# Kernel optimization log

Measured on AMD Instinct MI355X. Metric: run time of the kernel, lower is better.

## Reference

```python
import jax, jax.numpy as jnp
import numpy as np

B, S, D_MODEL, H, D = 2, 2048, 1024, 16, 64
SCALE = 1.0 / float(np.sqrt(D))


def setup_inputs() -> dict:
    key = jax.random.key(0)
    ks = jax.random.split(key, 5)
    x = jax.random.normal(ks[0], (B, S, D_MODEL), jnp.float32)
    qkv_w = jax.random.normal(ks[1], (3 * H * D, D_MODEL), jnp.float32) * 0.02
    out_w = jax.random.normal(ks[2], (D_MODEL, H * D), jnp.float32) * 0.02
    bias_p = jax.random.uniform(ks[3], (H, 1, 1), jnp.float32) * 2.0  # torch.rand(...)*2
    bias_a = jax.random.uniform(ks[4], (H, 1, 1), jnp.float32)
    # standard geometric RoPE frequencies over d_head//2 = 32 channels
    rope_freqs = 10000.0 ** (-jnp.arange(D // 2, dtype=jnp.float32) / (D // 2))
    return {"x": x, "qkv_w": qkv_w, "out_w": out_w,
            "bias_p": bias_p, "bias_a": bias_a, "rope_freqs": rope_freqs}


def _rope(t, c, s):
    # t: [B,H,S,d]; c,s: [1,1,S,d/2]. Split-half rotation as in apply_rope.
    d2 = t.shape[-1] // 2
    t1, t2 = t[..., :d2], t[..., d2:]
    return jnp.concatenate([t1 * c - t2 * s, t1 * s + t2 * c], axis=-1)


def reference(x, qkv_w, out_w, bias_p, bias_a, rope_freqs):
    Bb, Ss, _ = x.shape
    qkv = (x @ qkv_w.T).reshape(Bb, Ss, 3, H, D)
    q = qkv[:, :, 0].transpose(0, 2, 1, 3)  # [B,H,S,d]
    k = qkv[:, :, 1].transpose(0, 2, 1, 3)
    v = qkv[:, :, 2].transpose(0, 2, 1, 3)
    pos = jnp.arange(Ss, dtype=jnp.float32)
    ang = pos[:, None] * rope_freqs[None, :]                 # [S, d/2]
    c = jnp.cos(ang)[None, None]
    s = jnp.sin(ang)[None, None]
    q = _rope(q, c, s)
    k = _rope(k, c, s)
    scores = jnp.einsum('bhqd,bhkd->bhqk', q, k) * SCALE     # [B,H,S,S]
    p = jnp.maximum(bias_p, 0.01)                            # clamp(min=0.01)
    a = jnp.maximum(bias_a, 0.01)
    dist = jnp.abs(pos[None, :] - pos[:, None])              # [S,S]
    kb = -p * jnp.log1p(a * dist)                            # [H,S,S]
    attn = jax.nn.softmax(scores + kb[None], axis=-1)
    out = jnp.einsum('bhqk,bhkd->bhqd', attn, v)             # [B,H,S,d]
    out = out.transpose(0, 2, 1, 3).reshape(Bb, Ss, H * D)
    return out @ out_w.T
```

## Files before the change

### kernel.cpp

```cpp
#include <hip/hip_runtime.h>
#include <math.h>

#define BATCH  2
#define SEQ    2048
#define DMODEL 1024
#define NH     16
#define HD     64
#define NQKV   3072
#define ROWS   (BATCH*SEQ)

typedef unsigned short u16;
typedef __bf16 bf16x8 __attribute__((ext_vector_type(8)));
typedef float  f32x4  __attribute__((ext_vector_type(4)));

typedef const __attribute__((address_space(1))) void* gptr_t;
typedef __attribute__((address_space(3))) void* lptr_t;

__device__ __forceinline__ void gload16(lptr_t l, const void* g) {
    __builtin_amdgcn_global_load_lds((gptr_t)g, l, 16, 0, 0);
}

__device__ __forceinline__ u16 f2bf(float f) {
    unsigned int u = __float_as_uint(f);
    u += 0x7FFFu + ((u >> 16) & 1u);
    return (u16)(u >> 16);
}
__device__ __forceinline__ float bf2f(u16 v) {
    return __uint_as_float(((unsigned int)v) << 16);
}

__global__ void f2bf_kernel(const float* __restrict__ in, u16* __restrict__ out, int n)
{
    int i = (blockIdx.x * 256 + threadIdx.x) * 4;
    if (i >= n) return;
    float4 v = *(const float4*)(in + i);
    u16 o[4] = { f2bf(v.x), f2bf(v.y), f2bf(v.z), f2bf(v.w) };
    *(uint2*)(out + i) = *(const uint2*)o;
}

__global__ void bias_table_kernel(const float* __restrict__ bias_p,
                                  const float* __restrict__ bias_a,
                                  float* __restrict__ kb)
{
    int idx = blockIdx.x * 256 + threadIdx.x;
    int h = idx >> 11;
    int d = idx & (SEQ - 1);
    float p = fmaxf(bias_p[h], 0.01f);
    float a = fmaxf(bias_a[h], 0.01f);
    kb[idx] = -p * log1pf(a * (float)d);
}

__global__ void rope_table_kernel(const float* __restrict__ freqs, float* __restrict__ tab)
{
    int idx = blockIdx.x * 256 + threadIdx.x;
    int s = idx >> 5, d = idx & 31;
    float sn, cs;
    sincosf((float)s * freqs[d], &sn, &cs);
    tab[idx * 2]     = cs;
    tab[idx * 2 + 1] = sn;
}

template<bool BF16OUT>
__global__ __launch_bounds__(256) void gemm_bf16(
    const u16* __restrict__ A, const u16* __restrict__ B,
    void* __restrict__ Cout, int M, int N, int K)
{
    __shared__ __align__(16) u16 As[128][32];
    __shared__ __align__(16) u16 Bs[128][32];
    const int tid  = threadIdx.x;
    const int wave = tid >> 6, lane = tid & 63;
    const int quad = lane >> 4, l16 = lane & 15;
    const int wrow = (wave >> 1) * 64, wcol = (wave & 1) * 64;
    const int bm = blockIdx.x * 128, bn = blockIdx.y * 128;

    const int srow = lane >> 2;
    const int scol = ((lane & 3) ^ (srow & 3)) * 8;
    const int fsw = (quad ^ (l16 & 3)) * 8;

    f32x4 acc[4][4];
#pragma unroll
    for (int i = 0; i < 4; ++i)
#pragma unroll
        for (int j = 0; j < 4; ++j) acc[i][j] = (f32x4){0.f,0.f,0.f,0.f};

    const u16* Ag0 = A + (size_t)(bm + wave*32 + srow)      * K + scol;
    const u16* Ag1 = A + (size_t)(bm + wave*32 + 16 + srow) * K + scol;
    const u16* Bg0 = B + (size_t)(bn + wave*32 + srow)      * K + scol;
    const u16* Bg1 = B + (size_t)(bn + wave*32 + 16 + srow) * K + scol;

    for (int k0 = 0; k0 < K; k0 += 32) {
        __syncthreads();
        gload16((lptr_t)&As[wave*32][0],      Ag0 + k0);
        gload16((lptr_t)&As[wave*32 + 16][0], Ag1 + k0);
        gload16((lptr_t)&Bs[wave*32][0],      Bg0 + k0);
        gload16((lptr_t)&Bs[wave*32 + 16][0], Bg1 + k0);
        __syncthreads();
        bf16x8 af[4], bfr[4];
#pragma unroll
        for (int i = 0; i < 4; ++i)
            af[i] = *(const bf16x8*)&As[wrow + i*16 + l16][fsw];
#pragma unroll
        for (int j = 0; j < 4; ++j)
            bfr[j] = *(const bf16x8*)&Bs[wcol + j*16 + l16][fsw];
#pragma unroll
        for (int i = 0; i < 4; ++i)
#pragma unroll
            for (int j = 0; j < 4; ++j)
                acc[i][j] = __builtin_amdgcn_mfma_f32_16x16x32_bf16(af[i], bfr[j], acc[i][j], 0, 0, 0);
    }

#pragma unroll
    for (int i = 0; i < 4; ++i)
#pragma unroll
        for (int j = 0; j < 4; ++j) {
            int col = bn + wcol + j*16 + l16;
#pragma unroll
            for (int r = 0; r < 4; ++r) {
                int row = bm + wrow + i*16 + quad*4 + r;
                if (BF16OUT) ((u16*)Cout)[(size_t)row * N + col] = f2bf(acc[i][j][r]);
                else         ((float*)Cout)[(size_t)row * N + col] = acc[i][j][r];
            }
        }
}

__global__ __launch_bounds__(256) void qkv_convert(
    const u16* __restrict__ qkv_bf, const float* __restrict__ cs_tab,
    u16* __restrict__ Qb, u16* __restrict__ Kb, u16* __restrict__ Vt)
{
    __shared__ __align__(16) u16 Vtile[64][72];
    const int tid = threadIdx.x;
    const int r = tid >> 2, c = tid & 3;
    const int s0 = blockIdx.x * 64, h = blockIdx.y, b = blockIdx.z;
    const int s = s0 + r;
    const u16* src = qkv_bf + (size_t)(b * SEQ + s) * NQKV + h * HD;
    const size_t hb = (size_t)(b * NH + h) * SEQ * HD;

    *(uint4*)&Vtile[r][c*16]     = *(const uint4*)(src + 2*NH*HD + c*16);
    *(uint4*)&Vtile[r][c*16 + 8] = *(const uint4*)(src + 2*NH*HD + c*16 + 8);

    {
        const u16* m = src + ((c < 2) ? 0 : NH*HD);
        const int d1 = (c & 1) * 16;
        u16 x1[16], x2[16];
        *(uint4*)&x1[0] = *(const uint4*)(m + d1);
        *(uint4*)&x1[8] = *(const uint4*)(m + d1 + 8);
        *(uint4*)&x2[0] = *(const uint4*)(m + d1 + 32);
        *(uint4*)&x2[8] = *(const uint4*)(m + d1 + 40);
        const float* ct = cs_tab + ((size_t)s * 32 + d1) * 2;
        const float sc = (c < 2) ? 0.125f : 1.0f;
        u16 y1[16], y2[16];
#pragma unroll
        for (int u = 0; u < 16; ++u) {
            float cs = ct[u*2], sn = ct[u*2 + 1];
            float a = bf2f(x1[u]), bq = bf2f(x2[u]);
            y1[u] = f2bf((a * cs - bq * sn) * sc);
            y2[u] = f2bf((a * sn + bq * cs) * sc);
        }
        u16* dst = ((c < 2) ? Qb : Kb) + hb + (size_t)s * HD + d1;
        *(uint4*)(dst)      = *(const uint4*)&y1[0];
        *(uint4*)(dst + 8)  = *(const uint4*)&y1[8];
        *(uint4*)(dst + 32) = *(const uint4*)&y2[0];
        *(uint4*)(dst + 40) = *(const uint4*)&y2[8];
    }
    __syncthreads();

    u16 vv[16];
#pragma unroll
    for (int u = 0; u < 16; ++u) vv[u] = Vtile[c*16 + u][r];
    u16* dst = Vt + hb + (size_t)r * SEQ + s0 + c*16;
    *(uint4*)(dst)     = *(const uint4*)&vv[0];
    *(uint4*)(dst + 8) = *(const uint4*)&vv[8];
}

__global__ __launch_bounds__(256) void attn_mfma(
    const u16* __restrict__ Qb, const u16* __restrict__ Kb,
    const u16* __restrict__ Vt, const float* __restrict__ kbt,
    u16* __restrict__ attn_bf)
{
    __shared__ __align__(16) u16 Ks[64][64];
    __shared__ __align__(16) u16 Vs[64][64];
    __shared__ __align__(16) u16 Ps[64][72];
    __shared__ float bs_[128];

    const int tid = threadIdx.x;
    const int wave = tid >> 6, lane = tid & 63;
    const int quad = lane >> 4, l16 = lane & 15;
    const int q0 = blockIdx.x * 64, h = blockIdx.y, b = blockIdx.z;

    const u16* Qh = Qb + (size_t)(b * NH + h) * SEQ * HD;
    const u16* Kh = Kb + (size_t)(b * NH + h) * SEQ * HD;
    const u16* Vh = Vt + (size_t)(b * NH + h) * HD * SEQ;
    const float* kbh = kbt + h * SEQ;

    const int qrow = q0 + wave * 16 + l16;
    const bf16x8 qf0 = *(const bf16x8*)(Qh + (size_t)qrow * HD + quad * 8);
    const bf16x8 qf1 = *(const bf16x8*)(Qh + (size_t)qrow * HD + 32 + quad * 8);

    const int srow = lane >> 3;
    const int scol = ((lane & 7) ^ srow) * 8;
    const u16* Kg0 = Kh + (size_t)(wave*16 + srow)     * HD + scol;
    const u16* Kg1 = Kh + (size_t)(wave*16 + 8 + srow) * HD + scol;
    const u16* Vg0 = Vh + (size_t)(wave*16 + srow)     * SEQ + scol;
    const u16* Vg1 = Vh + (size_t)(wave*16 + 8 + srow) * SEQ + scol;
    const int sw = (quad ^ (l16 & 7)) * 8;

    float l_part[4] = {0.f, 0.f, 0.f, 0.f};
    f32x4 o[4];
#pragma unroll
    for (int j = 0; j < 4; ++j) o[j] = (f32x4){0.f,0.f,0.f,0.f};

    for (int kt = 0; kt < SEQ / 64; ++kt) {
        const int k0 = kt * 64;
        __syncthreads();
        gload16((lptr_t)&Ks[wave*16][0],     Kg0 + (size_t)k0 * HD);
        gload16((lptr_t)&Ks[wave*16 + 8][0], Kg1 + (size_t)k0 * HD);
        gload16((lptr_t)&Vs[wave*16][0],     Vg0 + k0);
        gload16((lptr_t)&Vs[wave*16 + 8][0], Vg1 + k0);
        int dq = q0 - k0; if (dq < 0) dq = -dq;
        const int lo = (dq <= 63) ? 0 : dq - 63;
        if (tid < 128) {
            int idx = lo + tid;
            bs_[tid] = kbh[idx < SEQ ? idx : SEQ - 1];
        }
        __syncthreads();

        f32x4 sc[4];
#pragma unroll
        for (int j = 0; j < 4; ++j) {
            bf16x8 kf0 = *(const bf16x8*)&Ks[j*16 + l16][sw];
            bf16x8 kf1 = *(const bf16x8*)&Ks[j*16 + l16][sw ^ 32];
            f32x4 z = (f32x4){0.f,0.f,0.f,0.f};
            z = __builtin_amdgcn_mfma_f32_16x16x32_bf16(qf0, kf0, z, 0, 0, 0);
            sc[j] = __builtin_amdgcn_mfma_f32_16x16x32_bf16(qf1, kf1, z, 0, 0, 0);
        }

#pragma unroll
        for (int r = 0; r < 4; ++r) {
            const int qidx = q0 + wave * 16 + quad * 4 + r;
            float e[4];
#pragma unroll
            for (int j = 0; j < 4; ++j) {
                int kidx = k0 + j * 16 + l16;
                int dist = qidx - kidx; if (dist < 0) dist = -dist;
                e[j] = __expf(sc[j][r] + bs_[dist - lo]);
                Ps[wave*16 + quad*4 + r][j*16 + l16] = f2bf(e[j]);
            }
            l_part[r] += (e[0] + e[1]) + (e[2] + e[3]);
        }

        bf16x8 pf0 = *(const bf16x8*)&Ps[wave*16 + l16][quad*8];
        bf16x8 pf1 = *(const bf16x8*)&Ps[wave*16 + l16][32 + quad*8];
#pragma unroll
        for (int j = 0; j < 4; ++j) {
            bf16x8 vf0 = *(const bf16x8*)&Vs[j*16 + l16][sw];
            bf16x8 vf1 = *(const bf16x8*)&Vs[j*16 + l16][sw ^ 32];
            o[j] = __builtin_amdgcn_mfma_f32_16x16x32_bf16(pf0, vf0, o[j], 0, 0, 0);
            o[j] = __builtin_amdgcn_mfma_f32_16x16x32_bf16(pf1, vf1, o[j], 0, 0, 0);
        }
    }

#pragma unroll
    for (int r = 0; r < 4; ++r) {
#pragma unroll
        for (int off = 1; off < 16; off <<= 1)
            l_part[r] += __shfl_xor(l_part[r], off);
        float inv = 1.0f / l_part[r];
        int row = q0 + wave * 16 + quad * 4 + r;
        u16* dst = attn_bf + (size_t)(b * SEQ + row) * DMODEL + h * HD;
#pragma unroll
        for (int j = 0; j < 4; ++j)
            dst[j*16 + l16] = f2bf(o[j][r] * inv);
    }
}

extern "C" void kernel_launch(void* const* d_in, const int* in_sizes, int n_in,
                              void* d_out, int out_size, void* d_ws, size_t ws_size,
                              hipStream_t stream)
{
    (void)in_sizes; (void)n_in; (void)out_size; (void)ws_size;
    const float* x      = (const float*)d_in[0];
    const float* qkv_w  = (const float*)d_in[1];
    const float* out_w  = (const float*)d_in[2];
    const float* bias_p = (const float*)d_in[3];
    const float* bias_a = (const float*)d_in[4];
    const float* freqs  = (const float*)d_in[5];
    float* out = (float*)d_out;

    char* ws = (char*)d_ws;
    u16*   qkv_bf  = (u16*)ws;
    u16*   attn_bf = (u16*)ws;
    u16*   x_bf    = (u16*)(ws + 25165824);
    u16*   Qb      = x_bf;
    u16*   w1_bf   = (u16*)(ws + 33554432);
    u16*   w2_bf   = (u16*)(ws + 39845888);
    u16*   Kb      = (u16*)(ws + 41943040);
    u16*   Vt      = (u16*)(ws + 50331648);
    float* kbt     = (float*)(ws + 58720256);
    float* cs_tab  = (float*)(ws + 58720256 + 131072);

    f2bf_kernel<<<dim3(ROWS*DMODEL/1024), 256, 0, stream>>>(x, x_bf, ROWS*DMODEL);
    f2bf_kernel<<<dim3(NQKV*DMODEL/1024), 256, 0, stream>>>(qkv_w, w1_bf, NQKV*DMODEL);
    f2bf_kernel<<<dim3(DMODEL*DMODEL/1024), 256, 0, stream>>>(out_w, w2_bf, DMODEL*DMODEL);
    rope_table_kernel<<<dim3(SEQ*32/256), 256, 0, stream>>>(freqs, cs_tab);
    bias_table_kernel<<<dim3(NH*SEQ/256), 256, 0, stream>>>(bias_p, bias_a, kbt);

    gemm_bf16<true><<<dim3(ROWS/128, NQKV/128), 256, 0, stream>>>(x_bf, w1_bf, qkv_bf, ROWS, NQKV, DMODEL);
    qkv_convert<<<dim3(SEQ/64, NH, BATCH), 256, 0, stream>>>(qkv_bf, cs_tab, Qb, Kb, Vt);
    attn_mfma<<<dim3(SEQ/64, NH, BATCH), 256, 0, stream>>>(Qb, Kb, Vt, kbt, attn_bf);
    gemm_bf16<false><<<dim3(ROWS/128, DMODEL/128), 256, 0, stream>>>(attn_bf, w2_bf, out, ROWS, DMODEL, DMODEL);
}
```

Before: 248.3 us.

## Restructure attention: split keys across waves, exp2 with multiplicative bias table, keep P in registers

The attention kernel is reorganised so each wave takes a 16-key slice of every K tile for all 64 queries, computing S^T. The probabilities stay in registers and feed the PV MFMA directly instead of going through a shared-memory P tile. Folding log2(e) into the Q scale allows exp2, and the distance bias becomes a precomputed multiplicative table exp(kb) stored as packed bf16, which removes an add and an exp per element. Because each wave now holds a partial output for all queries, results are combined with LDS atomicAdds at the end. The three f32-to-bf16 conversion kernels are merged into one launch; the costs are extra register pressure from o[4][4] and a bf16-precision bias weight.

```diff
diff --git a/kernel.cpp b/kernel.cpp
--- a/kernel.cpp
+++ b/kernel.cpp
@@ -8,9 +8,12 @@
 #define HD     64
 #define NQKV   3072
 #define ROWS   (BATCH*SEQ)
+#define QSCALE 0.18033688f
 
 typedef unsigned short u16;
+typedef unsigned int   u32;
 typedef __bf16 bf16x8 __attribute__((ext_vector_type(8)));
+typedef short  s16x4  __attribute__((ext_vector_type(4)));
 typedef float  f32x4  __attribute__((ext_vector_type(4)));
 
 typedef const __attribute__((address_space(1))) void* gptr_t;
@@ -28,26 +31,70 @@
 __device__ __forceinline__ float bf2f(u16 v) {
     return __uint_as_float(((unsigned int)v) << 16);
 }
-
-__global__ void f2bf_kernel(const float* __restrict__ in, u16* __restrict__ out, int n)
+__device__ __forceinline__ u32 pk2(float lo, float hi) {
+#if __has_builtin(__builtin_amdgcn_cvt_pk_bf16_f32)
+    typedef __bf16 bf16x2 __attribute__((ext_vector_type(2)));
+    union { bf16x2 v; u32 u; } cv;
+    cv.v = __builtin_amdgcn_cvt_pk_bf16_f32(lo, hi);
+    return cv.u;
+#else
+    return (u32)f2bf(lo) | ((u32)f2bf(hi) << 16);
+#endif
+}
+__device__ __forceinline__ float fexp2(float x) {
+#if __has_builtin(__builtin_amdgcn_exp2f)
+    return __builtin_amdgcn_exp2f(x);
+#else
+    return exp2f(x);
+#endif
+}
+
+#if __has_builtin(__builtin_amdgcn_mfma_f32_16x16x16_bf16)
+typedef __bf16 bf16x4 __attribute__((ext_vector_type(4)));
+__device__ __forceinline__ f32x4 pv_mfma(u32 v01, u32 v23, u32 p01, u32 p23, f32x4 c) {
+    union { uint2 u; bf16x4 v; } a, b;
+    a.u = make_uint2(v01, v23); b.u = make_uint2(p01, p23);
+    return __builtin_amdgcn_mfma_f32_16x16x16_bf16(a.v, b.v, c, 0, 0, 0);
+}
+#define PV_K16 1
+#elif __has_builtin(__builtin_amdgcn_mfma_f32_16x16x16bf16_1k)
+__device__ __forceinline__ f32x4 pv_mfma(u32 v01, u32 v23, u32 p01, u32 p23, f32x4 c) {
+    union { uint2 u; s16x4 v; } a, b;
+    a.u = make_uint2(v01, v23); b.u = make_uint2(p01, p23);
+    return __builtin_amdgcn_mfma_f32_16x16x16bf16_1k(a.v, b.v, c, 0, 0, 0);
+}
+#define PV_K16 1
+#else
+#define PV_K16 0
+#endif
+
+__global__ void f2bf3_kernel(const float* __restrict__ a, int na,
+                             const float* __restrict__ b, int nb,
+                             const float* __restrict__ c, int nc,
+                             u16* __restrict__ oa, u16* __restrict__ ob,
+                             u16* __restrict__ oc)
 {
     int i = (blockIdx.x * 256 + threadIdx.x) * 4;
-    if (i >= n) return;
-    float4 v = *(const float4*)(in + i);
+    const float* s; u16* d; int base;
+    if (i < na)                { s = a; d = oa; base = i; }
+    else if (i < na + nb)      { s = b; d = ob; base = i - na; }
+    else if (i < na + nb + nc) { s = c; d = oc; base = i - na - nb; }
+    else return;
+    float4 v = *(const float4*)(s + base);
     u16 o[4] = { f2bf(v.x), f2bf(v.y), f2bf(v.z), f2bf(v.w) };
-    *(uint2*)(out + i) = *(const uint2*)o;
-}
-
-__global__ void bias_table_kernel(const float* __restrict__ bias_p,
-                                  const float* __restrict__ bias_a,
-                                  float* __restrict__ kb)
+    *(uint2*)(d + base) = *(const uint2*)o;
+}
+
+__global__ void wtab_kernel(const float* __restrict__ bias_p,
+                            const float* __restrict__ bias_a,
+                            float* __restrict__ wtab)
 {
     int idx = blockIdx.x * 256 + threadIdx.x;
     int h = idx >> 11;
     int d = idx & (SEQ - 1);
     float p = fmaxf(bias_p[h], 0.01f);
     float a = fmaxf(bias_a[h], 0.01f);
-    kb[idx] = -p * log1pf(a * (float)d);
+    wtab[idx] = __expf(-p * log1pf(a * (float)d));
 }
 
 __global__ void rope_table_kernel(const float* __restrict__ freqs, float* __restrict__ tab)
@@ -147,7 +194,7 @@
         *(uint4*)&x2[0] = *(const uint4*)(m + d1 + 32);
         *(uint4*)&x2[8] = *(const uint4*)(m + d1 + 40);
         const float* ct = cs_tab + ((size_t)s * 32 + d1) * 2;
-        const float sc = (c < 2) ? 0.125f : 1.0f;
+        const float sc = (c < 2) ? QSCALE : 1.0f;
         u16 y1[16], y2[16];
 #pragma unroll
         for (int u = 0; u < 16; ++u) {
@@ -174,13 +221,13 @@
 
 __global__ __launch_bounds__(256) void attn_mfma(
     const u16* __restrict__ Qb, const u16* __restrict__ Kb,
-    const u16* __restrict__ Vt, const float* __restrict__ kbt,
+    const u16* __restrict__ Vt, const float* __restrict__ wtab,
     u16* __restrict__ attn_bf)
 {
-    __shared__ __align__(16) u16 Ks[64][64];
-    __shared__ __align__(16) u16 Vs[64][64];
-    __shared__ __align__(16) u16 Ps[64][72];
-    __shared__ float bs_[128];
+    __shared__ __align__(16) char smem[17408];
+    u16* Ks  = (u16*)smem;
+    u16* Vs  = (u16*)(smem + 8192);
+    u32* ws2 = (u32*)(smem + 16384);
 
     const int tid = threadIdx.x;
     const int wave = tid >> 6, lane = tid & 63;
@@ -190,11 +237,15 @@
     const u16* Qh = Qb + (size_t)(b * NH + h) * SEQ * HD;
     const u16* Kh = Kb + (size_t)(b * NH + h) * SEQ * HD;
     const u16* Vh = Vt + (size_t)(b * NH + h) * HD * SEQ;
-    const float* kbh = kbt + h * SEQ;
-
-    const int qrow = q0 + wave * 16 + l16;
-    const bf16x8 qf0 = *(const bf16x8*)(Qh + (size_t)qrow * HD + quad * 8);
-    const bf16x8 qf1 = *(const bf16x8*)(Qh + (size_t)qrow * HD + 32 + quad * 8);
+    const float* wh = wtab + h * SEQ;
+
+    bf16x8 qf0[4], qf1[4];
+#pragma unroll
+    for (int qj = 0; qj < 4; ++qj) {
+        const u16* qr = Qh + (size_t)(q0 + qj*16 + l16) * HD + quad * 8;
+        qf0[qj] = *(const bf16x8*)qr;
+        qf1[qj] = *(const bf16x8*)(qr + 32);
+    }
 
     const int srow = lane >> 3;
     const int scol = ((lane & 7) ^ srow) * 8;
@@ -202,74 +253,115 @@
     const u16* Kg1 = Kh + (size_t)(wave*16 + 8 + srow) * HD + scol;
     const u16* Vg0 = Vh + (size_t)(wave*16 + srow)     * SEQ + scol;
     const u16* Vg1 = Vh + (size_t)(wave*16 + 8 + srow) * SEQ + scol;
-    const int sw = (quad ^ (l16 & 7)) * 8;
-
-    float l_part[4] = {0.f, 0.f, 0.f, 0.f};
-    f32x4 o[4];
-#pragma unroll
-    for (int j = 0; j < 4; ++j) o[j] = (f32x4){0.f,0.f,0.f,0.f};
+
+    const int sw  = (quad ^ (l16 & 7)) * 8;
+    const int mb0 = 63 + l16 - wave*16 - quad*4 - 3;
+
+    float l_p[4] = {0.f, 0.f, 0.f, 0.f};
+    f32x4 o[4][4];
+#pragma unroll
+    for (int di = 0; di < 4; ++di)
+#pragma unroll
+        for (int qj = 0; qj < 4; ++qj) o[di][qj] = (f32x4){0.f,0.f,0.f,0.f};
 
     for (int kt = 0; kt < SEQ / 64; ++kt) {
         const int k0 = kt * 64;
         __syncthreads();
-        gload16((lptr_t)&Ks[wave*16][0],     Kg0 + (size_t)k0 * HD);
-        gload16((lptr_t)&Ks[wave*16 + 8][0], Kg1 + (size_t)k0 * HD);
-        gload16((lptr_t)&Vs[wave*16][0],     Vg0 + k0);
-        gload16((lptr_t)&Vs[wave*16 + 8][0], Vg1 + k0);
-        int dq = q0 - k0; if (dq < 0) dq = -dq;
-        const int lo = (dq <= 63) ? 0 : dq - 63;
+        gload16((lptr_t)&Ks[(wave*16)*64],     Kg0 + (size_t)k0 * HD);
+        gload16((lptr_t)&Ks[(wave*16 + 8)*64], Kg1 + (size_t)k0 * HD);
+        gload16((lptr_t)&Vs[(wave*16)*64],     Vg0 + k0);
+        gload16((lptr_t)&Vs[(wave*16 + 8)*64], Vg1 + k0);
         if (tid < 128) {
-            int idx = lo + tid;
-            bs_[tid] = kbh[idx < SEQ ? idx : SEQ - 1];
+            int i0 = (q0 - k0 - 63) + tid;
+            int a0 = i0 < 0 ? -i0 : i0;  if (a0 > SEQ-1) a0 = SEQ-1;
+            int i1 = i0 + 1;
+            int a1 = i1 < 0 ? -i1 : i1;  if (a1 > SEQ-1) a1 = SEQ-1;
+            ws2[tid] = pk2(wh[a0], wh[a1]);
         }
         __syncthreads();
 
-        f32x4 sc[4];
-#pragma unroll
-        for (int j = 0; j < 4; ++j) {
-            bf16x8 kf0 = *(const bf16x8*)&Ks[j*16 + l16][sw];
-            bf16x8 kf1 = *(const bf16x8*)&Ks[j*16 + l16][sw ^ 32];
+        bf16x8 kf0 = *(const bf16x8*)&Ks[(wave*16 + l16)*64 + sw];
+        bf16x8 kf1 = *(const bf16x8*)&Ks[(wave*16 + l16)*64 + (sw ^ 32)];
+        u32 pp[4][2];
+#pragma unroll
+        for (int qj = 0; qj < 4; ++qj) {
             f32x4 z = (f32x4){0.f,0.f,0.f,0.f};
-            z = __builtin_amdgcn_mfma_f32_16x16x32_bf16(qf0, kf0, z, 0, 0, 0);
-            sc[j] = __builtin_amdgcn_mfma_f32_16x16x32_bf16(qf1, kf1, z, 0, 0, 0);
-        }
-
-#pragma unroll
-        for (int r = 0; r < 4; ++r) {
-            const int qidx = q0 + wave * 16 + quad * 4 + r;
-            float e[4];
-#pragma unroll
-            for (int j = 0; j < 4; ++j) {
-                int kidx = k0 + j * 16 + l16;
-                int dist = qidx - kidx; if (dist < 0) dist = -dist;
-                e[j] = __expf(sc[j][r] + bs_[dist - lo]);
-                Ps[wave*16 + quad*4 + r][j*16 + l16] = f2bf(e[j]);
+            z = __builtin_amdgcn_mfma_f32_16x16x32_bf16(kf0, qf0[qj], z, 0, 0, 0);
+            z = __builtin_amdgcn_mfma_f32_16x16x32_bf16(kf1, qf1[qj], z, 0, 0, 0);
+            const int mbase = mb0 + qj*16;
+            u32 pA = ws2[mbase], pB = ws2[mbase + 2];
+            float w3 = __uint_as_float(pA << 16);
+            float w2 = __uint_as_float(pA & 0xffff0000u);
+            float w1 = __uint_as_float(pB << 16);
+            float w0 = __uint_as_float(pB & 0xffff0000u);
+            float e0 = fexp2(z[0]) * w0, e1 = fexp2(z[1]) * w1;
+            float e2 = fexp2(z[2]) * w2, e3 = fexp2(z[3]) * w3;
+            l_p[qj] += (e0 + e1) + (e2 + e3);
+            pp[qj][0] = pk2(e0, e1);
+            pp[qj][1] = pk2(e2, e3);
+        }
+
+#if PV_K16
+#pragma unroll
+        for (int di = 0; di < 4; ++di) {
+            const int row = di*16 + l16;
+            const int c   = 2*wave + (quad >> 1);
+            const int off = ((c ^ (row & 7)) * 8) + (quad & 1) * 4;
+            uint2 vv = *(const uint2*)&Vs[row*64 + off];
+#pragma unroll
+            for (int qj = 0; qj < 4; ++qj)
+                o[di][qj] = pv_mfma(vv.x, vv.y, pp[qj][0], pp[qj][1], o[di][qj]);
+        }
+#else
+#pragma unroll
+        for (int di = 0; di < 4; ++di) {
+            const int row = di*16 + l16;
+            union { uint4 u; bf16x8 v; } va;
+            if (quad < 2) {
+                const int c = 2*wave + quad;
+                va.u = *(const uint4*)&Vs[row*64 + ((c ^ (row & 7)) * 8)];
+            } else va.u = make_uint4(0,0,0,0);
+#pragma unroll
+            for (int qj = 0; qj < 4; ++qj) {
+                u32 s1a = __shfl_down(pp[qj][0], 16), s1b = __shfl_down(pp[qj][1], 16);
+                u32 s2a = __shfl_down(pp[qj][0], 32), s2b = __shfl_down(pp[qj][1], 32);
+                union { uint4 u; bf16x8 v; } pb;
+                if (quad == 0)      pb.u = make_uint4(pp[qj][0], pp[qj][1], s1a, s1b);
+                else if (quad == 1) pb.u = make_uint4(s1a, s1b, s2a, s2b);
+                else                pb.u = make_uint4(0,0,0,0);
+                o[di][qj] = __builtin_amdgcn_mfma_f32_16x16x32_bf16(va.v, pb.v, o[di][qj], 0, 0, 0);
             }
-            l_part[r] += (e[0] + e[1]) + (e[2] + e[3]);
-        }
-
-        bf16x8 pf0 = *(const bf16x8*)&Ps[wave*16 + l16][quad*8];
-        bf16x8 pf1 = *(const bf16x8*)&Ps[wave*16 + l16][32 + quad*8];
-#pragma unroll
-        for (int j = 0; j < 4; ++j) {
-            bf16x8 vf0 = *(const bf16x8*)&Vs[j*16 + l16][sw];
-            bf16x8 vf1 = *(const bf16x8*)&Vs[j*16 + l16][sw ^ 32];
-            o[j] = __builtin_amdgcn_mfma_f32_16x16x32_bf16(pf0, vf0, o[j], 0, 0, 0);
-            o[j] = __builtin_amdgcn_mfma_f32_16x16x32_bf16(pf1, vf1, o[j], 0, 0, 0);
-        }
+        }
+#endif
     }
 
-#pragma unroll
-    for (int r = 0; r < 4; ++r) {
-#pragma unroll
-        for (int off = 1; off < 16; off <<= 1)
-            l_part[r] += __shfl_xor(l_part[r], off);
-        float inv = 1.0f / l_part[r];
-        int row = q0 + wave * 16 + quad * 4 + r;
-        u16* dst = attn_bf + (size_t)(b * SEQ + row) * DMODEL + h * HD;
-#pragma unroll
-        for (int j = 0; j < 4; ++j)
-            dst[j*16 + l16] = f2bf(o[j][r] * inv);
+    __syncthreads();
+    float* Red = (float*)smem;
+    float* ls  = Red + 64*66;
+    for (int i = tid; i < 64*66 + 64; i += 256) Red[i] = 0.f;
+    __syncthreads();
+#pragma unroll
+    for (int qj = 0; qj < 4; ++qj)
+        atomicAdd(&ls[qj*16 + l16], l_p[qj]);
+#pragma unroll
+    for (int di = 0; di < 4; ++di)
+#pragma unroll
+        for (int qj = 0; qj < 4; ++qj)
+#pragma unroll
+            for (int r = 0; r < 4; ++r)
+                atomicAdd(&Red[(di*16 + quad*4 + r)*66 + qj*16 + l16], o[di][qj][r]);
+    __syncthreads();
+
+    {
+        const int q = tid >> 2, dc = (tid & 3) * 16;
+        float inv = 1.0f / ls[q];
+        u16 ov[16];
+#pragma unroll
+        for (int u = 0; u < 16; ++u)
+            ov[u] = f2bf(Red[(dc + u)*66 + q] * inv);
+        u16* dst = attn_bf + (size_t)(b * SEQ + q0 + q) * DMODEL + h * HD + dc;
+        *(uint4*)(dst)     = *(const uint4*)&ov[0];
+        *(uint4*)(dst + 8) = *(const uint4*)&ov[8];
     }
 }
 
@@ -295,17 +387,17 @@
     u16*   w2_bf   = (u16*)(ws + 39845888);
     u16*   Kb      = (u16*)(ws + 41943040);
     u16*   Vt      = (u16*)(ws + 50331648);
-    float* kbt     = (float*)(ws + 58720256);
+    float* wtab    = (float*)(ws + 58720256);
     float* cs_tab  = (float*)(ws + 58720256 + 131072);
 
-    f2bf_kernel<<<dim3(ROWS*DMODEL/1024), 256, 0, stream>>>(x, x_bf, ROWS*DMODEL);
-    f2bf_kernel<<<dim3(NQKV*DMODEL/1024), 256, 0, stream>>>(qkv_w, w1_bf, NQKV*DMODEL);
-    f2bf_kernel<<<dim3(DMODEL*DMODEL/1024), 256, 0, stream>>>(out_w, w2_bf, DMODEL*DMODEL);
+    const int na = ROWS*DMODEL, nb = NQKV*DMODEL, nc = DMODEL*DMODEL;
+    f2bf3_kernel<<<dim3((na+nb+nc)/1024), 256, 0, stream>>>(x, na, qkv_w, nb, out_w, nc,
+                                                            x_bf, w1_bf, w2_bf);
     rope_table_kernel<<<dim3(SEQ*32/256), 256, 0, stream>>>(freqs, cs_tab);
-    bias_table_kernel<<<dim3(NH*SEQ/256), 256, 0, stream>>>(bias_p, bias_a, kbt);
+    wtab_kernel<<<dim3(NH*SEQ/256), 256, 0, stream>>>(bias_p, bias_a, wtab);
 
     gemm_bf16<true><<<dim3(ROWS/128, NQKV/128), 256, 0, stream>>>(x_bf, w1_bf, qkv_bf, ROWS, NQKV, DMODEL);
     qkv_convert<<<dim3(SEQ/64, NH, BATCH), 256, 0, stream>>>(qkv_bf, cs_tab, Qb, Kb, Vt);
-    attn_mfma<<<dim3(SEQ/64, NH, BATCH), 256, 0, stream>>>(Qb, Kb, Vt, kbt, attn_bf);
+    attn_mfma<<<dim3(SEQ/64, NH, BATCH), 256, 0, stream>>>(Qb, Kb, Vt, wtab, attn_bf);
     gemm_bf16<false><<<dim3(ROWS/128, DMODEL/128), 256, 0, stream>>>(attn_bf, w2_bf, out, ROWS, DMODEL, DMODEL);
 }
```

Result: slower. 323.3 us (+30.2%).
